# Performance work log

Measured on AMD Instinct MI355X. Metric: run time of the kernel, lower is better.

Reference implementation:

```python
import jax, jax.numpy as jnp
import numpy as np

NUM_HEADS = 8


def _mc_linear(x, W, b):
    # Per-channel linear over the feature (h) dim.
    # x: (b,c,h,w), W: (c,f,h), b: (c,f,1) -> (b,c,f,w)
    return jnp.einsum('bchw,cfh->bcfw', x, W) + b


def setup_inputs() -> dict:
    key = jax.random.key(0)
    ks = jax.random.split(key, 9)
    b, c, f, w = 2, 8, 256, 1024
    s = 1.0 / np.sqrt(f).astype(np.float32)
    d = {'x': jax.random.normal(ks[0], (b, c, f, w), jnp.float32)}
    for i, name in enumerate(['q', 'k', 'v', 'o']):
        d['W' + name] = jax.random.normal(ks[1 + 2 * i], (c, f, f), jnp.float32) * s
        d['b' + name] = jax.random.normal(ks[2 + 2 * i], (c, f, 1), jnp.float32) * 0.01
    return d


def reference(x, Wq, bq, Wk, bk, Wv, bv, Wo, bo):
    b, c, h, w = x.shape
    hd = h // NUM_HEADS
    # projections -> (b,c,f,w), then to (b,c,heads,w,hd) / (b,c,heads,hd,w)
    q = _mc_linear(x, Wq, bq).transpose(0, 1, 3, 2).reshape(b, c, w, NUM_HEADS, hd).transpose(0, 1, 3, 2, 4)
    k = _mc_linear(x, Wk, bk).transpose(0, 1, 3, 2).reshape(b, c, w, NUM_HEADS, hd).transpose(0, 1, 3, 4, 2)
    v = _mc_linear(x, Wv, bv).transpose(0, 1, 3, 2).reshape(b, c, w, NUM_HEADS, hd).transpose(0, 1, 3, 2, 4)
    qk = jnp.matmul(q, k) / jnp.sqrt(jnp.asarray(h, x.dtype))  # (b,c,heads,w,w); note scale uses h, per source
    a = jnp.matmul(jax.nn.softmax(qk, axis=-1), v)             # (b,c,heads,w,hd)
    a = a.transpose(0, 1, 3, 2, 4).reshape(b, c, w, h).transpose(0, 1, 3, 2)  # (b,c,h,w)
    out = _mc_linear(a, Wo, bo)
    return out, qk
```

## Files before the change

### kernel.cpp

```cpp
#include <hip/hip_runtime.h>
#include <hip/hip_bf16.h>

#define BC 16
#define HH 256
#define WW 1024
#define NH 8
#define HD 32
#define PST 72

typedef __attribute__((ext_vector_type(8))) short bf16x8;
typedef __attribute__((ext_vector_type(4))) float f32x4;

static __device__ __forceinline__ unsigned short f2bu(float f) {
    __hip_bfloat16 h = __float2bfloat16(f);
    unsigned short r;
    __builtin_memcpy(&r, &h, 2);
    return r;
}

__global__ __launch_bounds__(256) void cast_fused(
    const float* __restrict__ x, __hip_bfloat16* __restrict__ xT,
    const float* __restrict__ w0, const float* __restrict__ w1,
    const float* __restrict__ w2, const float* __restrict__ w3,
    __hip_bfloat16* __restrict__ o0, __hip_bfloat16* __restrict__ o1,
    __hip_bfloat16* __restrict__ o2, __hip_bfloat16* __restrict__ o3) {
    if (blockIdx.z == 16) {
        const float* src = w0;
        __hip_bfloat16* dst = o0;
        float wscale = 0.0625f;
        if (blockIdx.y == 1) { src = w1; dst = o1; wscale = 1.0f; }
        else if (blockIdx.y == 2) { src = w2; dst = o2; wscale = 1.0f; }
        else if (blockIdx.y == 3) { src = w3; dst = o3; wscale = 1.0f; }
        const int base = blockIdx.x * 256 + threadIdx.x;
#pragma unroll
        for (int i = 0; i < 32; ++i) {
            const long t = (long)base + (long)i * 4096;
            float4 v = ((const float4*)src)[t];
            ushort4 o = make_ushort4(f2bu(v.x * wscale), f2bu(v.y * wscale),
                                     f2bu(v.z * wscale), f2bu(v.w * wscale));
            ((ushort4*)dst)[t] = o;
        }
        return;
    }
    __shared__ float tile[64][65];
    const int bc = blockIdx.z;
    const int h0 = blockIdx.y * 64, w0t = blockIdx.x * 64;
    const float* xp = x + ((long)bc * HH + h0) * WW + w0t;
    const int w4 = threadIdx.x & 15, hr = threadIdx.x >> 4;
#pragma unroll
    for (int p = 0; p < 4; ++p) {
        const int h = hr + p * 16;
        float4 v = *(const float4*)(xp + (long)h * WW + w4 * 4);
        tile[h][w4 * 4 + 0] = v.x;
        tile[h][w4 * 4 + 1] = v.y;
        tile[h][w4 * 4 + 2] = v.z;
        tile[h][w4 * 4 + 3] = v.w;
    }
    __syncthreads();
    __hip_bfloat16* xo = xT + ((long)bc * WW + w0t) * HH + h0;
    const int hq = threadIdx.x & 15, wq = threadIdx.x >> 4;
#pragma unroll
    for (int p = 0; p < 4; ++p) {
        const int w = wq + p * 16;
        ushort4 o = make_ushort4(f2bu(tile[hq * 4 + 0][w]), f2bu(tile[hq * 4 + 1][w]),
                                 f2bu(tile[hq * 4 + 2][w]), f2bu(tile[hq * 4 + 3][w]));
        *(ushort4*)(xo + (long)w * HH + hq * 4) = o;
    }
}

template <int MI, int NI, int OUTF32>
static __device__ __forceinline__ void gemm_body(
    const __hip_bfloat16* __restrict__ Ap, int lda,
    const __hip_bfloat16* __restrict__ Bp, int ldb,
    char* __restrict__ Cp, int ldc,
    const float* __restrict__ bp, int biasMode, float bmul,
    int m0, int n0, int lane) {
    const int lr = lane & 15, kl = (lane >> 4) * 8;

    const __hip_bfloat16* ap = Ap + (long)(m0 + lr) * lda + kl;
    const __hip_bfloat16* bpp = Bp + (long)(n0 + lr) * ldb + kl;

    f32x4 acc[MI][NI] = {};
    bf16x8 afA[MI], bfA[NI], afB[MI], bfB[NI];
#pragma unroll
    for (int i = 0; i < MI; ++i) afA[i] = *(const bf16x8*)(ap + (long)i * 16 * lda);
#pragma unroll
    for (int j = 0; j < NI; ++j) bfA[j] = *(const bf16x8*)(bpp + (long)j * 16 * ldb);

#pragma unroll
    for (int kk = 0; kk < 8; ++kk) {
        const int kn = (kk + 1) * 32;
        if ((kk & 1) == 0) {
            if (kn < HH) {
#pragma unroll
                for (int i = 0; i < MI; ++i)
                    afB[i] = *(const bf16x8*)(ap + (long)i * 16 * lda + kn);
#pragma unroll
                for (int j = 0; j < NI; ++j)
                    bfB[j] = *(const bf16x8*)(bpp + (long)j * 16 * ldb + kn);
            }
#pragma unroll
            for (int i = 0; i < MI; ++i)
#pragma unroll
                for (int j = 0; j < NI; ++j)
                    acc[i][j] = __builtin_amdgcn_mfma_f32_16x16x32_bf16(
                        afA[i], bfA[j], acc[i][j], 0, 0, 0);
        } else {
            if (kn < HH) {
#pragma unroll
                for (int i = 0; i < MI; ++i)
                    afA[i] = *(const bf16x8*)(ap + (long)i * 16 * lda + kn);
#pragma unroll
                for (int j = 0; j < NI; ++j)
                    bfA[j] = *(const bf16x8*)(bpp + (long)j * 16 * ldb + kn);
            }
#pragma unroll
            for (int i = 0; i < MI; ++i)
#pragma unroll
                for (int j = 0; j < NI; ++j)
                    acc[i][j] = __builtin_amdgcn_mfma_f32_16x16x32_bf16(
                        afB[i], bfB[j], acc[i][j], 0, 0, 0);
        }
    }

    const int col0 = lane & 15;
    const int rowg = (lane >> 4) * 4;
#pragma unroll
    for (int i = 0; i < MI; ++i) {
#pragma unroll
        for (int j = 0; j < NI; ++j) {
            const int n = n0 + j * 16 + col0;
            float addc = 0.0f;
            if (biasMode == 2) addc = bp[n] * bmul;
#pragma unroll
            for (int r = 0; r < 4; ++r) {
                const int m = m0 + i * 16 + rowg + r;
                float v = acc[i][j][r] + ((biasMode == 1) ? bp[m] : addc);
                if (OUTF32)
                    ((float*)Cp)[(long)m * ldc + n] = v;
                else
                    ((__hip_bfloat16*)Cp)[(long)m * ldc + n] = __float2bfloat16(v);
            }
        }
    }
}

__global__ __launch_bounds__(256, 3) void gemm_qkv(
    const __hip_bfloat16* __restrict__ xT,
    const __hip_bfloat16* __restrict__ wqb, const __hip_bfloat16* __restrict__ wkb,
    const __hip_bfloat16* __restrict__ wvb,
    __hip_bfloat16* __restrict__ Qt, __hip_bfloat16* __restrict__ Kt,
    __hip_bfloat16* __restrict__ Vm,
    const float* __restrict__ bq, const float* __restrict__ bk,
    const float* __restrict__ bv) {
    const int bc = blockIdx.z, ch = bc & 7, y = blockIdx.y;
    const int wave = threadIdx.x >> 6, lane = threadIdx.x & 63;
    const __hip_bfloat16* xb = xT + (long)bc * WW * HH;

    if (y < 2) {
        const __hip_bfloat16* wb = ((y == 0) ? wqb : wkb) + (long)ch * HH * HH;
        __hip_bfloat16* Cb = ((y == 0) ? Qt : Kt) + (long)bc * WW * HH;
        const float* bp = ((y == 0) ? bq : bk) + ch * HH;
        const float bmul = (y == 0) ? 0.0625f : 1.0f;
        const int bm = (blockIdx.x >> 1) * 128, bn = (blockIdx.x & 1) * 128;
        const int m0 = bm + (wave >> 1) * 64, n0 = bn + (wave & 1) * 64;
        gemm_body<4, 4, 0>(xb, HH, wb, HH, (char*)Cb, HH, bp, 2, bmul, m0, n0, lane);
    } else {
        const __hip_bfloat16* wb = wvb + (long)ch * HH * HH;
        __hip_bfloat16* Cb = Vm + (long)bc * HH * WW;
        const float* bp = bv + ch * HH;
        const int bm = (blockIdx.x >> 3) * 128, bn = (blockIdx.x & 7) * 128;
        const int m0 = bm + (wave >> 1) * 64, n0 = bn + (wave & 1) * 64;
        gemm_body<4, 4, 0>(wb, HH, xb, HH, (char*)Cb, WW, bp, 1, 1.0f, m0, n0, lane);
    }
}

__global__ __launch_bounds__(256, 2) void gemm_o(
    const __hip_bfloat16* __restrict__ wob, const __hip_bfloat16* __restrict__ At,
    float* __restrict__ out, const float* __restrict__ bo) {
    const int bc = blockIdx.z, ch = bc & 7;
    const int wave = threadIdx.x >> 6, lane = threadIdx.x & 63;
    const __hip_bfloat16* wb = wob + (long)ch * HH * HH;
    const __hip_bfloat16* ab = At + (long)bc * WW * HH;
    float* Cb = out + (long)bc * HH * WW;
    const float* bp = bo + ch * HH;
    const int bm = (blockIdx.x >> 4) * 128, bn = (blockIdx.x & 15) * 64;
    const int m0 = bm + (wave >> 1) * 64, n0 = bn + (wave & 1) * 32;
    gemm_body<4, 2, 1>(wb, HH, ab, HH, (char*)Cb, WW, bp, 1, 1.0f, m0, n0, lane);
}

static __device__ __forceinline__ void attn_body(
    const bf16x8 (&kc)[4], const bf16x8 (&vc)[2][2],
    bf16x8 (&kn)[4], bf16x8 (&vn)[2][2], bool pre, int wj,
    const bf16x8 (&qf)[2], __hip_bfloat16* __restrict__ pl,
    float* __restrict__ qkp,
    const __hip_bfloat16* __restrict__ Kb, const __hip_bfloat16* __restrict__ Vb,
    f32x4 (&oacc)[2][2], float (&lacc)[2][4],
    int lr, int g, int kl, int rowg) {
    const f32x4 zf = {0.0f, 0.0f, 0.0f, 0.0f};
    f32x4 s[2][4];
#pragma unroll
    for (int mf = 0; mf < 2; ++mf)
#pragma unroll
        for (int nf = 0; nf < 4; ++nf)
            s[mf][nf] = __builtin_amdgcn_mfma_f32_16x16x32_bf16(
                qf[mf], kc[nf], zf, 0, 0, 0);

    if (pre) {
#pragma unroll
        for (int nf = 0; nf < 4; ++nf)
            kn[nf] = *(const bf16x8*)(Kb + (long)(wj + 64 + nf * 16 + lr) * HH);
#pragma unroll
        for (int ks = 0; ks < 2; ++ks)
#pragma unroll
            for (int nf = 0; nf < 2; ++nf)
                vn[ks][nf] = *(const bf16x8*)(Vb + (long)(nf * 16 + lr) * WW +
                                              wj + 64 + ks * 32 + kl);
    }

#pragma unroll
    for (int mf = 0; mf < 2; ++mf)
#pragma unroll
        for (int r = 0; r < 4; ++r) {
            float* qr = qkp + (long)(mf * 16 + rowg + r) * WW + wj + lr;
#pragma unroll
            for (int nf = 0; nf < 4; ++nf)
                __builtin_nontemporal_store(s[mf][nf][r], qr + nf * 16);
        }

#pragma unroll
    for (int mf = 0; mf < 2; ++mf) {
        __hip_bfloat16* pw = pl + (long)(mf * 16 + rowg) * PST + lr;
#pragma unroll
        for (int nf = 0; nf < 4; ++nf)
#pragma unroll
            for (int r = 0; r < 4; ++r) {
                float p = __expf(s[mf][nf][r]);
                lacc[mf][r] += p;
                pw[r * PST + nf * 16] = __float2bfloat16(p);
            }
    }

#pragma unroll
    for (int ks = 0; ks < 2; ++ks) {
        bf16x8 pf[2];
#pragma unroll
        for (int mf = 0; mf < 2; ++mf)
            pf[mf] = *(const bf16x8*)(pl + (long)(mf * 16 + lr) * PST + ks * 32 + kl);
#pragma unroll
        for (int mf = 0; mf < 2; ++mf)
#pragma unroll
            for (int nf = 0; nf < 2; ++nf)
                oacc[mf][nf] = __builtin_amdgcn_mfma_f32_16x16x32_bf16(
                    pf[mf], vc[ks][nf], oacc[mf][nf], 0, 0, 0);
    }
}

__global__ __launch_bounds__(256) void attn_fused(
    const __hip_bfloat16* __restrict__ Qt, const __hip_bfloat16* __restrict__ Kt,
    const __hip_bfloat16* __restrict__ Vm, float* __restrict__ qk_out,
    __hip_bfloat16* __restrict__ At) {
    __shared__ __hip_bfloat16 P_lds[4][32 * PST];
    const int bc = blockIdx.z, head = blockIdx.y;
    const int wave = threadIdx.x >> 6, lane = threadIdx.x & 63;
    const int wi0 = blockIdx.x * 128 + wave * 32;
    const int lr = lane & 15, g = lane >> 4, kl = g * 8;
    const int rowg = g * 4;

    const __hip_bfloat16* Qb = Qt + (long)bc * WW * HH;
    bf16x8 qf[2];
#pragma unroll
    for (int mf = 0; mf < 2; ++mf)
        qf[mf] = *(const bf16x8*)(Qb + (long)(wi0 + mf * 16 + lr) * HH + head * HD + kl);

    const __hip_bfloat16* Kb = Kt + (long)bc * WW * HH + head * HD + kl;
    const __hip_bfloat16* Vb = Vm + ((long)bc * HH + head * HD) * WW;
    float* qkp = qk_out + (((long)bc * NH + head) * WW + wi0) * WW;

    f32x4 oacc[2][2] = {};
    float lacc[2][4] = {};
    __hip_bfloat16* pl = &P_lds[wave][0];

    bf16x8 kfA[4], kfB[4], vfA[2][2], vfB[2][2];
#pragma unroll
    for (int nf = 0; nf < 4; ++nf)
        kfA[nf] = *(const bf16x8*)(Kb + (long)(nf * 16 + lr) * HH);
#pragma unroll
    for (int ks = 0; ks < 2; ++ks)
#pragma unroll
        for (int nf = 0; nf < 2; ++nf)
            vfA[ks][nf] = *(const bf16x8*)(Vb + (long)(nf * 16 + lr) * WW +
                                           ks * 32 + kl);

    for (int it = 0; it < 8; ++it) {
        const int wj0 = it * 128;
        attn_body(kfA, vfA, kfB, vfB, true, wj0,
                  qf, pl, qkp, Kb, Vb, oacc, lacc, lr, g, kl, rowg);
        attn_body(kfB, vfB, kfA, vfA, (it < 7), wj0 + 64,
                  qf, pl, qkp, Kb, Vb, oacc, lacc, lr, g, kl, rowg);
    }

    float linv[2][4];
#pragma unroll
    for (int mf = 0; mf < 2; ++mf)
#pragma unroll
        for (int r = 0; r < 4; ++r) {
            float v = lacc[mf][r];
            v += __shfl_xor(v, 1);
            v += __shfl_xor(v, 2);
            v += __shfl_xor(v, 4);
            v += __shfl_xor(v, 8);
            linv[mf][r] = 1.0f / v;
        }

    __hip_bfloat16* Ao = At + (long)bc * WW * HH;
#pragma unroll
    for (int mf = 0; mf < 2; ++mf)
#pragma unroll
        for (int nf = 0; nf < 2; ++nf)
#pragma unroll
            for (int r = 0; r < 4; ++r) {
                float v = oacc[mf][nf][r] * linv[mf][r];
                Ao[(long)(wi0 + mf * 16 + rowg + r) * HH + head * HD + nf * 16 + lr] =
                    __float2bfloat16(v);
            }
}

extern "C" void kernel_launch(void* const* d_in, const int* in_sizes, int n_in,
                              void* d_out, int out_size, void* d_ws, size_t ws_size,
                              hipStream_t stream) {
    const float* x  = (const float*)d_in[0];
    const float* Wq = (const float*)d_in[1];
    const float* bq = (const float*)d_in[2];
    const float* Wk = (const float*)d_in[3];
    const float* bk = (const float*)d_in[4];
    const float* Wv = (const float*)d_in[5];
    const float* bv = (const float*)d_in[6];
    const float* Wo = (const float*)d_in[7];
    const float* bo = (const float*)d_in[8];

    float* out = (float*)d_out;
    float* qk  = out + (long)BC * HH * WW;

    char* ws = (char*)d_ws;
    __hip_bfloat16* xT  = (__hip_bfloat16*)(ws);
    __hip_bfloat16* wqb = (__hip_bfloat16*)(ws + 8388608);
    __hip_bfloat16* wkb = (__hip_bfloat16*)(ws + 9437184);
    __hip_bfloat16* wvb = (__hip_bfloat16*)(ws + 10485760);
    __hip_bfloat16* wob = (__hip_bfloat16*)(ws + 11534336);
    __hip_bfloat16* Qt  = (__hip_bfloat16*)(ws + 12582912);
    __hip_bfloat16* Kt  = (__hip_bfloat16*)(ws + 20971520);
    __hip_bfloat16* Vm  = (__hip_bfloat16*)(ws + 29360128);
    __hip_bfloat16* At  = (__hip_bfloat16*)(ws + 37748736);

    cast_fused<<<dim3(16, 4, 17), 256, 0, stream>>>(
        x, xT, Wq, Wk, Wv, Wo, wqb, wkb, wvb, wob);

    gemm_qkv<<<dim3(16, 3, BC), 256, 0, stream>>>(
        xT, wqb, wkb, wvb, Qt, Kt, Vm, bq, bk, bv);

    attn_fused<<<dim3(8, NH, BC), 256, 0, stream>>>(Qt, Kt, Vm, qk, At);

    gemm_o<<<dim3(32, 1, BC), 256, 0, stream>>>(wob, At, out, bo);

    (void)in_sizes; (void)n_in; (void)out_size; (void)ws_size;
}
```

Before: 200.7 us.

## Compute transposed QK tiles for vectorized qk stores and packed LDS writes

Swaps the MFMA operand order so each lane holds four consecutive key columns of one query row. This lets the fp32 qk output be written as 16-byte vector stores instead of scalar stores, and the bf16 probabilities be written to LDS as packed 32-bit pairs. The row-sum accumulator shrinks to one value per row fragment and is reduced across lane groups, then broadcast with shuffles. It relies on the transposed fragment layout matching the P-tile addressing used later by the PV MFMA.

```diff
diff --git a/kernel.cpp b/kernel.cpp
--- a/kernel.cpp
+++ b/kernel.cpp
@@ -16,6 +16,9 @@
     unsigned short r;
     __builtin_memcpy(&r, &h, 2);
     return r;
+}
+static __device__ __forceinline__ unsigned pack2(float a, float b) {
+    return (unsigned)f2bu(a) | ((unsigned)f2bu(b) << 16);
 }
 
 __global__ __launch_bounds__(256) void cast_fused(
@@ -195,16 +198,9 @@
     const bf16x8 (&qf)[2], __hip_bfloat16* __restrict__ pl,
     float* __restrict__ qkp,
     const __hip_bfloat16* __restrict__ Kb, const __hip_bfloat16* __restrict__ Vb,
-    f32x4 (&oacc)[2][2], float (&lacc)[2][4],
+    f32x4 (&oacc)[2][2], float (&lacc)[2],
     int lr, int g, int kl, int rowg) {
     const f32x4 zf = {0.0f, 0.0f, 0.0f, 0.0f};
-    f32x4 s[2][4];
-#pragma unroll
-    for (int mf = 0; mf < 2; ++mf)
-#pragma unroll
-        for (int nf = 0; nf < 4; ++nf)
-            s[mf][nf] = __builtin_amdgcn_mfma_f32_16x16x32_bf16(
-                qf[mf], kc[nf], zf, 0, 0, 0);
 
     if (pre) {
 #pragma unroll
@@ -218,35 +214,44 @@
                                               wj + 64 + ks * 32 + kl);
     }
 
+    f32x4 st[4][2];
+#pragma unroll
+    for (int nf = 0; nf < 4; ++nf)
+#pragma unroll
+        for (int mf = 0; mf < 2; ++mf)
+            st[nf][mf] = __builtin_amdgcn_mfma_f32_16x16x32_bf16(
+                kc[nf], qf[mf], zf, 0, 0, 0);
+
+#pragma unroll
+    for (int mf = 0; mf < 2; ++mf) {
+        unsigned* pw = (unsigned*)(pl + (long)(mf * 16 + lr) * PST + rowg);
+#pragma unroll
+        for (int nf = 0; nf < 4; ++nf) {
+            float p0 = __expf(st[nf][mf][0]);
+            float p1 = __expf(st[nf][mf][1]);
+            float p2 = __expf(st[nf][mf][2]);
+            float p3 = __expf(st[nf][mf][3]);
+            lacc[mf] += (p0 + p1) + (p2 + p3);
+            pw[nf * 8 + 0] = pack2(p0, p1);
+            pw[nf * 8 + 1] = pack2(p2, p3);
+        }
+    }
+
 #pragma unroll
     for (int mf = 0; mf < 2; ++mf)
 #pragma unroll
-        for (int r = 0; r < 4; ++r) {
-            float* qr = qkp + (long)(mf * 16 + rowg + r) * WW + wj + lr;
-#pragma unroll
-            for (int nf = 0; nf < 4; ++nf)
-                __builtin_nontemporal_store(s[mf][nf][r], qr + nf * 16);
-        }
-
-#pragma unroll
-    for (int mf = 0; mf < 2; ++mf) {
-        __hip_bfloat16* pw = pl + (long)(mf * 16 + rowg) * PST + lr;
-#pragma unroll
         for (int nf = 0; nf < 4; ++nf)
-#pragma unroll
-            for (int r = 0; r < 4; ++r) {
-                float p = __expf(s[mf][nf][r]);
-                lacc[mf][r] += p;
-                pw[r * PST + nf * 16] = __float2bfloat16(p);
-            }
-    }
+            __builtin_nontemporal_store(
+                st[nf][mf],
+                (f32x4*)(qkp + (long)(mf * 16 + lr) * WW + wj + nf * 16 + rowg));
 
 #pragma unroll
     for (int ks = 0; ks < 2; ++ks) {
         bf16x8 pf[2];
 #pragma unroll
         for (int mf = 0; mf < 2; ++mf)
-            pf[mf] = *(const bf16x8*)(pl + (long)(mf * 16 + lr) * PST + ks * 32 + kl);
+            pf[mf] = *(const bf16x8*)(pl + (long)(mf * 16 + lr) * PST +
+                                      ks * 32 + kl);
 #pragma unroll
         for (int mf = 0; mf < 2; ++mf)
 #pragma unroll
@@ -278,7 +283,7 @@
     float* qkp = qk_out + (((long)bc * NH + head) * WW + wi0) * WW;
 
     f32x4 oacc[2][2] = {};
-    float lacc[2][4] = {};
+    float lacc[2] = {0.0f, 0.0f};
     __hip_bfloat16* pl = &P_lds[wave][0];
 
     bf16x8 kfA[4], kfB[4], vfA[2][2], vfB[2][2];
@@ -300,18 +305,17 @@
                   qf, pl, qkp, Kb, Vb, oacc, lacc, lr, g, kl, rowg);
     }
 
+#pragma unroll
+    for (int mf = 0; mf < 2; ++mf) {
+        lacc[mf] += __shfl_xor(lacc[mf], 16);
+        lacc[mf] += __shfl_xor(lacc[mf], 32);
+    }
     float linv[2][4];
 #pragma unroll
     for (int mf = 0; mf < 2; ++mf)
 #pragma unroll
-        for (int r = 0; r < 4; ++r) {
-            float v = lacc[mf][r];
-            v += __shfl_xor(v, 1);
-            v += __shfl_xor(v, 2);
-            v += __shfl_xor(v, 4);
-            v += __shfl_xor(v, 8);
-            linv[mf][r] = 1.0f / v;
-        }
+        for (int r = 0; r < 4; ++r)
+            linv[mf][r] = 1.0f / __shfl(lacc[mf], rowg + r);
 
     __hip_bfloat16* Ao = At + (long)bc * WW * HH;
 #pragma unroll
```

Measured after the change: 217.8 us. 8.5% more time.
